# Kernel tuning notes

Measured on AMD Instinct MI355X. Metric: run time of the kernel, lower is better.

Reference implementation:

```python
import jax, jax.numpy as jnp
import numpy as np

B, T, I, H, S, L, F = 256, 365, 32, 256, 27, 7, 8  # batch, seq, input, hidden, static, output_len, future_input


def _lin(k, out_dim, in_dim):
    s = 1.0 / np.sqrt(in_dim)
    return jax.random.uniform(k, (out_dim, in_dim), jnp.float32, -s, s)


def setup_inputs() -> dict:
    key = jax.random.key(0)
    ks = jax.random.split(key, 32)
    d = {
        "x": jax.random.normal(ks[0], (B, T, I), jnp.float32),
        "static": jax.random.normal(ks[1], (B, S), jnp.float32),
        "future": jax.random.normal(ks[2], (B, L, F), jnp.float32),
        # layer 0 EA-LSTM cell
        "Wsh0": _lin(ks[3], H, S), "bsh0": jnp.zeros((H,), jnp.float32),
        "Wdg0": _lin(ks[4], 3 * H, I),
        "bdg0": jnp.concatenate([jnp.ones((H,), jnp.float32), jnp.zeros((2 * H,), jnp.float32)]),
        "Whg0": _lin(ks[5], 3 * H, H),
        # layer 1 EA-LSTM cell
        "Wsh1": _lin(ks[6], H, S), "bsh1": jnp.zeros((H,), jnp.float32),
        "Wdg1": _lin(ks[7], 3 * H, I),
        "bdg1": jnp.concatenate([jnp.ones((H,), jnp.float32), jnp.zeros((2 * H,), jnp.float32)]),
        "Whg1": _lin(ks[8], 3 * H, H),
        # hidden -> input projection between layers
        "Wp0": _lin(ks[9], I, H), "bp0": jnp.zeros((I,), jnp.float32),
        # projection head: Linear(H,H) -> ReLU -> Linear(H,L)
        "Wh1": _lin(ks[10], H, H), "bh1": jnp.zeros((H,), jnp.float32),
        "Wh2": _lin(ks[11], L, H), "bh2": jnp.zeros((L,), jnp.float32),
        # future forcing head: Linear(F*L,H) -> ReLU -> Linear(H,L)
        "Wf1": _lin(ks[12], H, F * L), "bf1": jnp.zeros((H,), jnp.float32),
        "Wf2": _lin(ks[13], L, H), "bf2": jnp.zeros((L,), jnp.float32),
    }
    return d


def _ealstm_layer(seq_tbi, static, Wsh, bsh, Wdg, bdg, Whg):
    """seq_tbi: [T,B,in]. Returns all hidden states [T,B,H]."""
    i_gate = jax.nn.sigmoid(static @ Wsh.T + bsh)  # [B,H], static input gate
    gates_x = jnp.einsum('tbi,gi->tbg', seq_tbi, Wdg) + bdg  # [T,B,3H]

    def step(carry, gx):
        h, c = carry
        gates = gx + h @ Whg.T
        f, o, g = jnp.split(gates, 3, axis=-1)
        f = jax.nn.sigmoid(f)
        o = jax.nn.sigmoid(o)
        g = jnp.tanh(g)
        c1 = f * c + i_gate * g
        h1 = o * jnp.tanh(c1)
        return (h1, c1), h1

    hB = seq_tbi.shape[1]
    init = (jnp.zeros((hB, Whg.shape[1]), seq_tbi.dtype),
            jnp.zeros((hB, Whg.shape[1]), seq_tbi.dtype))
    _, hs = jax.lax.scan(step, init, gates_x)
    return hs


def reference(x, static, future,
              Wsh0, bsh0, Wdg0, bdg0, Whg0,
              Wsh1, bsh1, Wdg1, bdg1, Whg1,
              Wp0, bp0, Wh1, bh1, Wh2, bh2,
              Wf1, bf1, Wf2, bf2):
    batch = x.shape[0]
    seq = jnp.swapaxes(x, 0, 1)  # [T,B,I]
    h0 = _ealstm_layer(seq, static, Wsh0, bsh0, Wdg0, bdg0, Whg0)  # [T,B,H]
    inp1 = jnp.einsum('tbh,ih->tbi', h0, Wp0) + bp0  # [T,B,I]
    h1 = _ealstm_layer(inp1, static, Wsh1, bsh1, Wdg1, bdg1, Whg1)
    final_h = h1[-1]  # [B,H]
    out = jax.nn.relu(final_h @ Wh1.T + bh1) @ Wh2.T + bh2  # [B,L]
    fut = jax.nn.relu(future.reshape(batch, -1) @ Wf1.T + bf1) @ Wf2.T + bf2
    return (out + fut)[..., None]  # [B,L,1]
```

## Files before the change

kernel.cpp:

```cpp
#include <hip/hip_runtime.h>
#include <math.h>

#define B_DIM 256
#define T_DIM 365
#define I_DIM 32
#define H_DIM 256
#define S_DIM 27
#define L_DIM 7
#define FL_DIM 56
#define G3 768
#define K_DIM 288
#define K2_DIM 144

typedef __attribute__((ext_vector_type(2))) _Float16 half2v;

__device__ __forceinline__ float fast_rcp(float x) { return __builtin_amdgcn_rcpf(x); }
__device__ __forceinline__ float sigm(float x) { return fast_rcp(1.0f + __expf(-x)); }
__device__ __forceinline__ float tanh_fast(float x) { return 1.0f - 2.0f * fast_rcp(1.0f + __expf(2.0f * x)); }

__device__ __forceinline__ float dot2(uint w, uint s, float acc) {
#if __has_builtin(__builtin_amdgcn_fdot2)
    return __builtin_amdgcn_fdot2(__builtin_bit_cast(half2v, w), __builtin_bit_cast(half2v, s), acc, false);
#else
    half2v a = __builtin_bit_cast(half2v, w), b = __builtin_bit_cast(half2v, s);
    return acc + (float)a.x * (float)b.x + (float)a.y * (float)b.y;
#endif
}

__device__ __forceinline__ ushort f16bits(float v) {
    _Float16 h = (_Float16)v;
    return __builtin_bit_cast(ushort, h);
}

__global__ void k_pack_w(const float* __restrict__ Wdg, const float* __restrict__ Whg,
                         uint* __restrict__ WTh) {
    int idx = blockIdx.x * 256 + threadIdx.x;
    if (idx >= K2_DIM * G3) return;
    int k2 = idx / G3, g = idx % G3;
    int k0 = 2 * k2, k1 = 2 * k2 + 1;
    float w0 = (k0 < I_DIM) ? Wdg[g * I_DIM + k0] : Whg[g * H_DIM + (k0 - I_DIM)];
    float w1 = (k1 < I_DIM) ? Wdg[g * I_DIM + k1] : Whg[g * H_DIM + (k1 - I_DIM)];
    half2v p; p.x = (_Float16)w0; p.y = (_Float16)w1;
    WTh[idx] = __builtin_bit_cast(uint, p);
}

__global__ void k_transpose(const float* __restrict__ in, float* __restrict__ out, int M, int N) {
    int idx = blockIdx.x * 256 + threadIdx.x;
    if (idx >= M * N) return;
    int n = idx / M, m = idx % M;
    out[idx] = in[m * N + n];
}

__global__ void k_igate(const float* __restrict__ st, const float* __restrict__ Wsh,
                        const float* __restrict__ bsh, float* __restrict__ ig) {
    __shared__ float s[S_DIM];
    int b = blockIdx.x, h = threadIdx.x;
    if (h < S_DIM) s[h] = st[b * S_DIM + h];
    __syncthreads();
    float a = bsh[h];
    for (int k = 0; k < S_DIM; ++k) a += s[k] * Wsh[h * S_DIM + k];
    ig[b * H_DIM + h] = sigm(a);
}

__global__ __launch_bounds__(768) void k_main(
    const float* __restrict__ x, const float* __restrict__ future,
    const uint* __restrict__ WTh0, const uint* __restrict__ WTh1,
    const float* __restrict__ bdg0, const float* __restrict__ bdg1,
    const float* __restrict__ ig0, const float* __restrict__ ig1,
    const float* __restrict__ WpT, const float* __restrict__ bp0,
    const float* __restrict__ Wh1T, const float* __restrict__ bh1,
    const float* __restrict__ Wh2, const float* __restrict__ bh2,
    const float* __restrict__ Wf1T, const float* __restrict__ bf1,
    const float* __restrict__ Wf2, const float* __restrict__ bf2,
    float* __restrict__ out) {
    __shared__ uint2 xq0[K2_DIM];
    __shared__ uint2 xq1[K2_DIM];
    __shared__ float pre0[3][2][H_DIM];
    __shared__ float pre1[3][2][H_DIM];
    __shared__ float hbuf[2][H_DIM];
    __shared__ float hbuf1[2][H_DIM];
    __shared__ float pbuf[4][64];
    __shared__ float futs[2][FL_DIM];

    const int t = threadIdx.x;
    const int r0 = blockIdx.x * 2;
    ushort* xq0h = (ushort*)xq0;
    ushort* xq1h = (ushort*)xq1;

    if (t < K2_DIM) { xq0[t] = make_uint2(0u, 0u); xq1[t] = make_uint2(0u, 0u); }
    __syncthreads();
    if (t < 64) {
        int row = t >> 5, i = t & 31;
        float v = x[(r0 + row) * (T_DIM * I_DIM) + i];
        xq0h[(i >> 1) * 4 + row * 2 + (i & 1)] = f16bits(v);
    }
    const float bia0 = bdg0[t], bia1 = bdg1[t];
    float ig00 = 0.f, ig01 = 0.f, ig10 = 0.f, ig11 = 0.f;
    float c00 = 0.f, c01 = 0.f, c10 = 0.f, c11 = 0.f;
    if (t < H_DIM) {
        ig00 = ig0[(r0 + 0) * H_DIM + t]; ig01 = ig0[(r0 + 1) * H_DIM + t];
        ig10 = ig1[(r0 + 0) * H_DIM + t]; ig11 = ig1[(r0 + 1) * H_DIM + t];
    }
    const int col = t & 255, which = t >> 8;
    const uint* w0p = WTh0 + t;
    const uint* w1p = WTh1 + t;
    __syncthreads();

    for (int ts = 0; ts < T_DIM; ++ts) {
        float a0 = bia0, a1 = bia0;
#pragma unroll 8
        for (int k2 = 0; k2 < K2_DIM; ++k2) {
            uint2 s = xq0[k2];
            uint w = w0p[k2 * G3];
            a0 = dot2(w, s.x, a0);
            a1 = dot2(w, s.y, a1);
        }
        pre0[which][0][col] = a0; pre0[which][1][col] = a1;
        __syncthreads();
        if (t < H_DIM) {
            float f0 = sigm(pre0[0][0][t]), f1 = sigm(pre0[0][1][t]);
            float o0 = sigm(pre0[1][0][t]), o1 = sigm(pre0[1][1][t]);
            float g0 = tanh_fast(pre0[2][0][t]), g1 = tanh_fast(pre0[2][1][t]);
            c00 = f0 * c00 + ig00 * g0; c01 = f1 * c01 + ig01 * g1;
            float h00 = o0 * tanh_fast(c00), h01 = o1 * tanh_fast(c01);
            hbuf[0][t] = h00; hbuf[1][t] = h01;
            int k = I_DIM + t, k2 = k >> 1;
            xq0h[k2 * 4 + (k & 1)] = f16bits(h00);
            xq0h[k2 * 4 + 2 + (k & 1)] = f16bits(h01);
        } else if (t >= 512 && t < 576 && ts + 1 < T_DIM) {
            int tt = t - 512, row = tt >> 5, i = tt & 31;
            float v = x[(r0 + row) * (T_DIM * I_DIM) + (ts + 1) * I_DIM + i];
            xq0h[(i >> 1) * 4 + row * 2 + (i & 1)] = f16bits(v);
        }
        __syncthreads();
        if (t >= 256 && t < 512) {
            int t2 = t - 256, i = t2 & 63, slice = t2 >> 6;
            int row = i >> 5, cp = i & 31;
            const float* hb = hbuf[row];
            const float* wp = WpT + cp;
            float acc = 0.f;
            int h0i = slice * 64;
#pragma unroll 8
            for (int h = h0i; h < h0i + 64; ++h) acc += hb[h] * wp[h * I_DIM];
            pbuf[slice][i] = acc;
        }
        __syncthreads();
        if (t < 32) {
            int row = t >> 4, jp = t & 15;
            int i0 = row * 32 + 2 * jp, i1 = i0 + 1;
            float v0 = pbuf[0][i0] + pbuf[1][i0] + pbuf[2][i0] + pbuf[3][i0] + bp0[2 * jp];
            float v1 = pbuf[0][i1] + pbuf[1][i1] + pbuf[2][i1] + pbuf[3][i1] + bp0[2 * jp + 1];
            half2v p; p.x = (_Float16)v0; p.y = (_Float16)v1;
            ((uint*)xq1)[jp * 2 + row] = __builtin_bit_cast(uint, p);
        }
        __syncthreads();
        a0 = bia1; a1 = bia1;
#pragma unroll 8
        for (int k2 = 0; k2 < K2_DIM; ++k2) {
            uint2 s = xq1[k2];
            uint w = w1p[k2 * G3];
            a0 = dot2(w, s.x, a0);
            a1 = dot2(w, s.y, a1);
        }
        pre1[which][0][col] = a0; pre1[which][1][col] = a1;
        __syncthreads();
        if (t < H_DIM) {
            float f0 = sigm(pre1[0][0][t]), f1 = sigm(pre1[0][1][t]);
            float o0 = sigm(pre1[1][0][t]), o1 = sigm(pre1[1][1][t]);
            float g0 = tanh_fast(pre1[2][0][t]), g1 = tanh_fast(pre1[2][1][t]);
            c10 = f0 * c10 + ig10 * g0; c11 = f1 * c11 + ig11 * g1;
            float h10 = o0 * tanh_fast(c10), h11 = o1 * tanh_fast(c11);
            hbuf1[0][t] = h10; hbuf1[1][t] = h11;
            int k = I_DIM + t, k2 = k >> 1;
            xq1h[k2 * 4 + (k & 1)] = f16bits(h10);
            xq1h[k2 * 4 + 2 + (k & 1)] = f16bits(h11);
        }
    }
    __syncthreads();

    if (t < 2 * FL_DIM) { int row = t / FL_DIM, k = t % FL_DIM; futs[row][k] = future[(r0 + row) * FL_DIM + k]; }
    if (t < H_DIM) {
        float a0 = bh1[t], a1 = bh1[t];
        for (int h = 0; h < H_DIM; ++h) {
            float w = Wh1T[h * H_DIM + t];
            a0 += w * hbuf1[0][h]; a1 += w * hbuf1[1][h];
        }
        pre0[0][0][t] = fmaxf(a0, 0.f); pre0[0][1][t] = fmaxf(a1, 0.f);
    }
    __syncthreads();
    if (t < H_DIM) {
        float b0 = bf1[t], b1 = bf1[t];
        for (int k = 0; k < FL_DIM; ++k) {
            float w = Wf1T[k * H_DIM + t];
            b0 += w * futs[0][k]; b1 += w * futs[1][k];
        }
        pre0[1][0][t] = fmaxf(b0, 0.f); pre0[1][1][t] = fmaxf(b1, 0.f);
    }
    __syncthreads();
    if (t < 2 * L_DIM) {
        int row = t / L_DIM, l = t % L_DIM;
        float acc = bh2[l] + bf2[l];
        for (int j = 0; j < H_DIM; ++j)
            acc += pre0[0][row][j] * Wh2[l * H_DIM + j] + pre0[1][row][j] * Wf2[l * H_DIM + j];
        out[(r0 + row) * L_DIM + l] = acc;
    }
}

extern "C" void kernel_launch(void* const* d_in, const int* in_sizes, int n_in,
                              void* d_out, int out_size, void* d_ws, size_t ws_size,
                              hipStream_t stream) {
    const float* x    = (const float*)d_in[0];
    const float* stat = (const float*)d_in[1];
    const float* fut  = (const float*)d_in[2];
    const float* Wsh0 = (const float*)d_in[3];
    const float* bsh0 = (const float*)d_in[4];
    const float* Wdg0 = (const float*)d_in[5];
    const float* bdg0 = (const float*)d_in[6];
    const float* Whg0 = (const float*)d_in[7];
    const float* Wsh1 = (const float*)d_in[8];
    const float* bsh1 = (const float*)d_in[9];
    const float* Wdg1 = (const float*)d_in[10];
    const float* bdg1 = (const float*)d_in[11];
    const float* Whg1 = (const float*)d_in[12];
    const float* Wp0  = (const float*)d_in[13];
    const float* bp0  = (const float*)d_in[14];
    const float* Wh1  = (const float*)d_in[15];
    const float* bh1  = (const float*)d_in[16];
    const float* Wh2  = (const float*)d_in[17];
    const float* bh2  = (const float*)d_in[18];
    const float* Wf1  = (const float*)d_in[19];
    const float* bf1  = (const float*)d_in[20];
    const float* Wf2  = (const float*)d_in[21];
    const float* bf2  = (const float*)d_in[22];

    float* ws   = (float*)d_ws;
    uint*  WTh0 = (uint*)ws;
    uint*  WTh1 = WTh0 + K2_DIM * G3;
    float* WpT  = (float*)(WTh1 + K2_DIM * G3);
    float* Wh1T = WpT + H_DIM * I_DIM;
    float* Wf1T = Wh1T + H_DIM * H_DIM;
    float* ig0  = Wf1T + FL_DIM * H_DIM;
    float* ig1  = ig0 + B_DIM * H_DIM;

    k_pack_w<<<(K2_DIM * G3 + 255) / 256, 256, 0, stream>>>(Wdg0, Whg0, WTh0);
    k_pack_w<<<(K2_DIM * G3 + 255) / 256, 256, 0, stream>>>(Wdg1, Whg1, WTh1);
    k_transpose<<<(I_DIM * H_DIM + 255) / 256, 256, 0, stream>>>(Wp0, WpT, I_DIM, H_DIM);
    k_transpose<<<(H_DIM * H_DIM + 255) / 256, 256, 0, stream>>>(Wh1, Wh1T, H_DIM, H_DIM);
    k_transpose<<<(H_DIM * FL_DIM + 255) / 256, 256, 0, stream>>>(Wf1, Wf1T, H_DIM, FL_DIM);
    k_igate<<<B_DIM, H_DIM, 0, stream>>>(stat, Wsh0, bsh0, ig0);
    k_igate<<<B_DIM, H_DIM, 0, stream>>>(stat, Wsh1, bsh1, ig1);
    k_main<<<B_DIM / 2, 768, 0, stream>>>(x, fut, WTh0, WTh1, bdg0, bdg1, ig0, ig1,
                                          WpT, bp0, Wh1T, bh1, Wh2, bh2, Wf1T, bf1, Wf2, bf2,
                                          (float*)d_out);
}
```

Measured before the change: 3.841 ms.

## Hoist layer-1 recurrent matvec alongside layer-0 and vectorize weight loads

The layer-1 recurrent term (Whg1·h1 from the previous step) only depends on the prior timestep, so it is now computed in the same loop as the layer-0 gates, leaving just the small 32-wide input projection after the inter-layer projection. Weights are repacked into 16-byte chunks so each thread issues uint4 loads covering four half2 pairs, and the per-row activation vectors are split into separate uint4 LDS arrays. This shortens the serial dependency chain per timestep and cuts the number of load instructions. It adds an extra barrier at the end of each step and changes the packed weight layout.

Result: faster. 3.572 ms (-7.0%).

```diff
diff --git a/kernel.cpp b/kernel.cpp
--- a/kernel.cpp
+++ b/kernel.cpp
@@ -9,8 +9,10 @@
 #define L_DIM 7
 #define FL_DIM 56
 #define G3 768
-#define K_DIM 288
-#define K2_DIM 144
+#define NC_A0 36
+#define NC_A1 32
+#define NC_A  68
+#define NC_B  4
 
 typedef __attribute__((ext_vector_type(2))) _Float16 half2v;
 
@@ -32,16 +34,39 @@
     return __builtin_bit_cast(ushort, h);
 }
 
-__global__ void k_pack_w(const float* __restrict__ Wdg, const float* __restrict__ Whg,
-                         uint* __restrict__ WTh) {
+__global__ void k_pack_A(const float* __restrict__ Wdg0, const float* __restrict__ Whg0,
+                         const float* __restrict__ Whg1, uint* __restrict__ WA) {
     int idx = blockIdx.x * 256 + threadIdx.x;
-    if (idx >= K2_DIM * G3) return;
-    int k2 = idx / G3, g = idx % G3;
-    int k0 = 2 * k2, k1 = 2 * k2 + 1;
-    float w0 = (k0 < I_DIM) ? Wdg[g * I_DIM + k0] : Whg[g * H_DIM + (k0 - I_DIM)];
-    float w1 = (k1 < I_DIM) ? Wdg[g * I_DIM + k1] : Whg[g * H_DIM + (k1 - I_DIM)];
+    if (idx >= NC_A * G3 * 4) return;
+    int j = idx & 3;
+    int g = (idx >> 2) % G3;
+    int c = idx / (4 * G3);
+    float w0, w1;
+    if (c < NC_A0) {
+        int k2 = 4 * c + j;
+        int k0 = 2 * k2, k1 = k0 + 1;
+        w0 = (k0 < I_DIM) ? Wdg0[g * I_DIM + k0] : Whg0[g * H_DIM + (k0 - I_DIM)];
+        w1 = (k1 < I_DIM) ? Wdg0[g * I_DIM + k1] : Whg0[g * H_DIM + (k1 - I_DIM)];
+    } else {
+        int k2 = 4 * (c - NC_A0) + j;
+        int k0 = 2 * k2, k1 = k0 + 1;
+        w0 = Whg1[g * H_DIM + k0];
+        w1 = Whg1[g * H_DIM + k1];
+    }
     half2v p; p.x = (_Float16)w0; p.y = (_Float16)w1;
-    WTh[idx] = __builtin_bit_cast(uint, p);
+    WA[idx] = __builtin_bit_cast(uint, p);
+}
+
+__global__ void k_pack_B(const float* __restrict__ Wdg1, uint* __restrict__ WB) {
+    int idx = blockIdx.x * 256 + threadIdx.x;
+    if (idx >= NC_B * G3 * 4) return;
+    int j = idx & 3;
+    int g = (idx >> 2) % G3;
+    int c = idx / (4 * G3);
+    int k2 = 4 * c + j;
+    int k0 = 2 * k2, k1 = k0 + 1;
+    half2v p; p.x = (_Float16)Wdg1[g * I_DIM + k0]; p.y = (_Float16)Wdg1[g * I_DIM + k1];
+    WB[idx] = __builtin_bit_cast(uint, p);
 }
 
 __global__ void k_transpose(const float* __restrict__ in, float* __restrict__ out, int M, int N) {
@@ -64,7 +89,7 @@
 
 __global__ __launch_bounds__(768) void k_main(
     const float* __restrict__ x, const float* __restrict__ future,
-    const uint* __restrict__ WTh0, const uint* __restrict__ WTh1,
+    const uint* __restrict__ WA, const uint* __restrict__ WB,
     const float* __restrict__ bdg0, const float* __restrict__ bdg1,
     const float* __restrict__ ig0, const float* __restrict__ ig1,
     const float* __restrict__ WpT, const float* __restrict__ bp0,
@@ -73,8 +98,9 @@
     const float* __restrict__ Wf1T, const float* __restrict__ bf1,
     const float* __restrict__ Wf2, const float* __restrict__ bf2,
     float* __restrict__ out) {
-    __shared__ uint2 xq0[K2_DIM];
-    __shared__ uint2 xq1[K2_DIM];
+    __shared__ uint4 xr0A[NC_A0], xr1A[NC_A0];
+    __shared__ uint4 hr0[NC_A1], hr1[NC_A1];
+    __shared__ uint4 xq1x0[NC_B], xq1x1[NC_B];
     __shared__ float pre0[3][2][H_DIM];
     __shared__ float pre1[3][2][H_DIM];
     __shared__ float hbuf[2][H_DIM];
@@ -84,15 +110,16 @@
 
     const int t = threadIdx.x;
     const int r0 = blockIdx.x * 2;
-    ushort* xq0h = (ushort*)xq0;
-    ushort* xq1h = (ushort*)xq1;
-
-    if (t < K2_DIM) { xq0[t] = make_uint2(0u, 0u); xq1[t] = make_uint2(0u, 0u); }
+
+    uint4 u4z = make_uint4(0u, 0u, 0u, 0u);
+    if (t < NC_A0) { xr0A[t] = u4z; xr1A[t] = u4z; }
+    if (t < NC_A1) { hr0[t] = u4z; hr1[t] = u4z; }
     __syncthreads();
     if (t < 64) {
         int row = t >> 5, i = t & 31;
         float v = x[(r0 + row) * (T_DIM * I_DIM) + i];
-        xq0h[(i >> 1) * 4 + row * 2 + (i & 1)] = f16bits(v);
+        if (row == 0) ((ushort*)xr0A)[i] = f16bits(v);
+        else          ((ushort*)xr1A)[i] = f16bits(v);
     }
     const float bia0 = bdg0[t], bia1 = bdg1[t];
     float ig00 = 0.f, ig01 = 0.f, ig10 = 0.f, ig11 = 0.f;
@@ -102,18 +129,32 @@
         ig10 = ig1[(r0 + 0) * H_DIM + t]; ig11 = ig1[(r0 + 1) * H_DIM + t];
     }
     const int col = t & 255, which = t >> 8;
-    const uint* w0p = WTh0 + t;
-    const uint* w1p = WTh1 + t;
     __syncthreads();
 
     for (int ts = 0; ts < T_DIM; ++ts) {
         float a0 = bia0, a1 = bia0;
+        float b0 = bia1, b1 = bia1;
+        {
+            const uint4* wa = (const uint4*)WA + t;
 #pragma unroll 8
-        for (int k2 = 0; k2 < K2_DIM; ++k2) {
-            uint2 s = xq0[k2];
-            uint w = w0p[k2 * G3];
-            a0 = dot2(w, s.x, a0);
-            a1 = dot2(w, s.y, a1);
+            for (int c = 0; c < NC_A0; ++c) {
+                uint4 w = wa[c * G3];
+                uint4 s0 = xr0A[c], s1 = xr1A[c];
+                a0 = dot2(w.x, s0.x, a0); a1 = dot2(w.x, s1.x, a1);
+                a0 = dot2(w.y, s0.y, a0); a1 = dot2(w.y, s1.y, a1);
+                a0 = dot2(w.z, s0.z, a0); a1 = dot2(w.z, s1.z, a1);
+                a0 = dot2(w.w, s0.w, a0); a1 = dot2(w.w, s1.w, a1);
+            }
+            const uint4* wh = (const uint4*)WA + NC_A0 * G3 + t;
+#pragma unroll 8
+            for (int c = 0; c < NC_A1; ++c) {
+                uint4 w = wh[c * G3];
+                uint4 s0 = hr0[c], s1 = hr1[c];
+                b0 = dot2(w.x, s0.x, b0); b1 = dot2(w.x, s1.x, b1);
+                b0 = dot2(w.y, s0.y, b0); b1 = dot2(w.y, s1.y, b1);
+                b0 = dot2(w.z, s0.z, b0); b1 = dot2(w.z, s1.z, b1);
+                b0 = dot2(w.w, s0.w, b0); b1 = dot2(w.w, s1.w, b1);
+            }
         }
         pre0[which][0][col] = a0; pre0[which][1][col] = a1;
         __syncthreads();
@@ -124,13 +165,13 @@
             c00 = f0 * c00 + ig00 * g0; c01 = f1 * c01 + ig01 * g1;
             float h00 = o0 * tanh_fast(c00), h01 = o1 * tanh_fast(c01);
             hbuf[0][t] = h00; hbuf[1][t] = h01;
-            int k = I_DIM + t, k2 = k >> 1;
-            xq0h[k2 * 4 + (k & 1)] = f16bits(h00);
-            xq0h[k2 * 4 + 2 + (k & 1)] = f16bits(h01);
+            ((ushort*)xr0A)[I_DIM + t] = f16bits(h00);
+            ((ushort*)xr1A)[I_DIM + t] = f16bits(h01);
         } else if (t >= 512 && t < 576 && ts + 1 < T_DIM) {
             int tt = t - 512, row = tt >> 5, i = tt & 31;
             float v = x[(r0 + row) * (T_DIM * I_DIM) + (ts + 1) * I_DIM + i];
-            xq0h[(i >> 1) * 4 + row * 2 + (i & 1)] = f16bits(v);
+            if (row == 0) ((ushort*)xr0A)[i] = f16bits(v);
+            else          ((ushort*)xr1A)[i] = f16bits(v);
         }
         __syncthreads();
         if (t >= 256 && t < 512) {
@@ -151,18 +192,24 @@
             float v0 = pbuf[0][i0] + pbuf[1][i0] + pbuf[2][i0] + pbuf[3][i0] + bp0[2 * jp];
             float v1 = pbuf[0][i1] + pbuf[1][i1] + pbuf[2][i1] + pbuf[3][i1] + bp0[2 * jp + 1];
             half2v p; p.x = (_Float16)v0; p.y = (_Float16)v1;
-            ((uint*)xq1)[jp * 2 + row] = __builtin_bit_cast(uint, p);
-        }
-        __syncthreads();
-        a0 = bia1; a1 = bia1;
-#pragma unroll 8
-        for (int k2 = 0; k2 < K2_DIM; ++k2) {
-            uint2 s = xq1[k2];
-            uint w = w1p[k2 * G3];
-            a0 = dot2(w, s.x, a0);
-            a1 = dot2(w, s.y, a1);
-        }
-        pre1[which][0][col] = a0; pre1[which][1][col] = a1;
+            uint pw = __builtin_bit_cast(uint, p);
+            if (row == 0) ((uint*)xq1x0)[jp] = pw;
+            else          ((uint*)xq1x1)[jp] = pw;
+        }
+        __syncthreads();
+        {
+            const uint4* wb = (const uint4*)WB + t;
+#pragma unroll 4
+            for (int c = 0; c < NC_B; ++c) {
+                uint4 w = wb[c * G3];
+                uint4 s0 = xq1x0[c], s1 = xq1x1[c];
+                b0 = dot2(w.x, s0.x, b0); b1 = dot2(w.x, s1.x, b1);
+                b0 = dot2(w.y, s0.y, b0); b1 = dot2(w.y, s1.y, b1);
+                b0 = dot2(w.z, s0.z, b0); b1 = dot2(w.z, s1.z, b1);
+                b0 = dot2(w.w, s0.w, b0); b1 = dot2(w.w, s1.w, b1);
+            }
+        }
+        pre1[which][0][col] = b0; pre1[which][1][col] = b1;
         __syncthreads();
         if (t < H_DIM) {
             float f0 = sigm(pre1[0][0][t]), f1 = sigm(pre1[0][1][t]);
@@ -171,12 +218,11 @@
             c10 = f0 * c10 + ig10 * g0; c11 = f1 * c11 + ig11 * g1;
             float h10 = o0 * tanh_fast(c10), h11 = o1 * tanh_fast(c11);
             hbuf1[0][t] = h10; hbuf1[1][t] = h11;
-            int k = I_DIM + t, k2 = k >> 1;
-            xq1h[k2 * 4 + (k & 1)] = f16bits(h10);
-            xq1h[k2 * 4 + 2 + (k & 1)] = f16bits(h11);
-        }
-    }
-    __syncthreads();
+            ((ushort*)hr0)[t] = f16bits(h10);
+            ((ushort*)hr1)[t] = f16bits(h11);
+        }
+        __syncthreads();
+    }
 
     if (t < 2 * FL_DIM) { int row = t / FL_DIM, k = t % FL_DIM; futs[row][k] = future[(r0 + row) * FL_DIM + k]; }
     if (t < H_DIM) {
@@ -234,22 +280,22 @@
     const float* bf2  = (const float*)d_in[22];
 
     float* ws   = (float*)d_ws;
-    uint*  WTh0 = (uint*)ws;
-    uint*  WTh1 = WTh0 + K2_DIM * G3;
-    float* WpT  = (float*)(WTh1 + K2_DIM * G3);
+    uint*  WA   = (uint*)ws;
+    uint*  WB   = WA + NC_A * G3 * 4;
+    float* WpT  = (float*)(WB + NC_B * G3 * 4);
     float* Wh1T = WpT + H_DIM * I_DIM;
     float* Wf1T = Wh1T + H_DIM * H_DIM;
     float* ig0  = Wf1T + FL_DIM * H_DIM;
     float* ig1  = ig0 + B_DIM * H_DIM;
 
-    k_pack_w<<<(K2_DIM * G3 + 255) / 256, 256, 0, stream>>>(Wdg0, Whg0, WTh0);
-    k_pack_w<<<(K2_DIM * G3 + 255) / 256, 256, 0, stream>>>(Wdg1, Whg1, WTh1);
+    k_pack_A<<<(NC_A * G3 * 4 + 255) / 256, 256, 0, stream>>>(Wdg0, Whg0, Whg1, WA);
+    k_pack_B<<<(NC_B * G3 * 4 + 255) / 256, 256, 0, stream>>>(Wdg1, WB);
     k_transpose<<<(I_DIM * H_DIM + 255) / 256, 256, 0, stream>>>(Wp0, WpT, I_DIM, H_DIM);
     k_transpose<<<(H_DIM * H_DIM + 255) / 256, 256, 0, stream>>>(Wh1, Wh1T, H_DIM, H_DIM);
     k_transpose<<<(H_DIM * FL_DIM + 255) / 256, 256, 0, stream>>>(Wf1, Wf1T, H_DIM, FL_DIM);
     k_igate<<<B_DIM, H_DIM, 0, stream>>>(stat, Wsh0, bsh0, ig0);
     k_igate<<<B_DIM, H_DIM, 0, stream>>>(stat, Wsh1, bsh1, ig1);
-    k_main<<<B_DIM / 2, 768, 0, stream>>>(x, fut, WTh0, WTh1, bdg0, bdg1, ig0, ig1,
+    k_main<<<B_DIM / 2, 768, 0, stream>>>(x, fut, WA, WB, bdg0, bdg1, ig0, ig1,
                                           WpT, bp0, Wh1T, bh1, Wh2, bh2, Wf1T, bf1, Wf2, bf2,
                                           (float*)d_out);
 }
```
